# Kernel tuning notes

Hardware: AMD Instinct MI355X
Metric: run time of the kernel (lower is better)

Reference implementation:

```python
import jax, jax.numpy as jnp
import numpy as np

N = 50000      # nodes
E = 800000     # edges (avg degree 16)
F_IN = 256     # in_feats
HID = 64       # hidden_dim (per-head out)
H = 4          # num heads (both layers)
NC = 23        # num_class
NEG_SLOPE = 0.2


def _gat_layer(h, W, attn_l, attn_r, bias, src, dst):
    # h: [N, F_in] -> out: [N, H*HID]; DGL GATConv math (no dropout)
    feat = (h @ W.T).reshape(-1, H, HID)                      # [N,H,D]
    el = jnp.einsum('nhd,hd->nh', feat, attn_l)               # [N,H]
    er = jnp.einsum('nhd,hd->nh', feat, attn_r)               # [N,H]
    e = jax.nn.leaky_relu(el[src] + er[dst], NEG_SLOPE)       # [E,H]
    # edge softmax over incoming edges of each dst node
    m = jax.ops.segment_max(e, dst, num_segments=N)           # [N,H]
    m = jnp.where(jnp.isfinite(m), m, 0.0)
    ex = jnp.exp(e - m[dst])                                  # [E,H]
    den = jax.ops.segment_sum(ex, dst, num_segments=N)        # [N,H]
    a = ex / jnp.maximum(den[dst], 1e-9)                      # [E,H]
    out = jax.ops.segment_sum(a[:, :, None] * feat[src], dst, num_segments=N)  # [N,H,D]
    out = out + bias.reshape(1, H, HID)
    return jax.nn.relu(out).reshape(-1, H * HID)


def setup_inputs() -> dict:
    key = jax.random.key(0)
    ks = jax.random.split(key, 18)
    s = 0.05
    emb = jax.random.normal(ks[4], (NC + 1, F_IN), jnp.float32) * s
    emb = emb.at[NC].set(0.0)  # padding_idx row
    return {
        'features': jax.random.normal(ks[0], (N, F_IN), jnp.float32),
        'input_labels': jax.random.randint(ks[1], (N,), 0, NC + 1),
        'src': jax.random.randint(ks[2], (E,), 0, N),
        'dst': jax.random.randint(ks[3], (E,), 0, N),
        'emb': emb,
        'le_W1': jax.random.normal(ks[5], (4 * F_IN, 2 * F_IN), jnp.float32) * s,
        'le_b1': jnp.zeros((4 * F_IN,), jnp.float32),
        'ln_g': jnp.ones((4 * F_IN,), jnp.float32),
        'ln_b': jnp.zeros((4 * F_IN,), jnp.float32),
        'le_W2': jax.random.normal(ks[6], (F_IN, 4 * F_IN), jnp.float32) * s,
        'le_b2': jnp.zeros((F_IN,), jnp.float32),
        'W1': jax.random.normal(ks[7], (H * HID, F_IN), jnp.float32) * s,
        'al1': jax.random.normal(ks[8], (H, HID), jnp.float32) * s,
        'ar1': jax.random.normal(ks[9], (H, HID), jnp.float32) * s,
        'b1': jnp.zeros((H * HID,), jnp.float32),
        'W2': jax.random.normal(ks[10], (H * HID, H * HID), jnp.float32) * s,
        'al2': jax.random.normal(ks[11], (H, HID), jnp.float32) * s,
        'ar2': jax.random.normal(ks[12], (H, HID), jnp.float32) * s,
        'b2': jnp.zeros((H * HID,), jnp.float32),
    }


def reference(features, emb, le_W1, le_b1, ln_g, ln_b, le_W2, le_b2,
              W1, al1, ar1, b1, W2, al2, ar2, b2,
              input_labels, src, dst):
    # label embedding + 2-layer MLP with LayerNorm (label_embed_layer)
    lab = emb[input_labels]                                   # [N,F_IN]
    x = jnp.concatenate([features, lab], axis=-1)             # [N,2F]
    x = x @ le_W1.T + le_b1                                   # [N,4F]
    mu = jnp.mean(x, axis=-1, keepdims=True)
    var = jnp.var(x, axis=-1, keepdims=True)
    x = (x - mu) * jax.lax.rsqrt(var + 1e-5) * ln_g + ln_b
    x = jax.nn.relu(x)
    h = x @ le_W2.T + le_b2                                   # [N,F_IN]
    h = _gat_layer(h, W1, al1, ar1, b1, src, dst)             # [N,H*HID]
    h = _gat_layer(h, W2, al2, ar2, b2, src, dst)             # [N,H*HID]
    return h
```

## Files before the change

kernel.cpp:

```cpp
#include <hip/hip_runtime.h>
#include <hip/hip_bf16.h>

typedef unsigned short u16;
typedef unsigned int   u32;

#define N_NODES 50000
#define N_EDGES 800000

using s16x8 = __attribute__((ext_vector_type(8))) short;
using f32x4 = __attribute__((ext_vector_type(4))) float;

__device__ __forceinline__ float bf2f(u16 u) {
  u32 x = ((u32)u) << 16;
  return __uint_as_float(x);
}
__device__ __forceinline__ u16 f2bf(float f) {
  u32 x = __float_as_uint(f);
  u32 r = (x + 0x7fffu + ((x >> 16) & 1u)) >> 16;
  return (u16)r;
}
__device__ __forceinline__ s16x8 cvt8_f32(const float* p) {
  const float4 f0 = *reinterpret_cast<const float4*>(p);
  const float4 f1 = *reinterpret_cast<const float4*>(p + 4);
  s16x8 v;
  v[0] = (short)f2bf(f0.x); v[1] = (short)f2bf(f0.y);
  v[2] = (short)f2bf(f0.z); v[3] = (short)f2bf(f0.w);
  v[4] = (short)f2bf(f1.x); v[5] = (short)f2bf(f1.y);
  v[6] = (short)f2bf(f1.z); v[7] = (short)f2bf(f1.w);
  return v;
}

__global__ __launch_bounds__(64)
void detect_dtype(const u16* __restrict__ feats, int* __restrict__ flag)
{
  const int lane = threadIdx.x;
  const u16 u = feats[lane * 2];
  const int ex = (u >> 7) & 0xFF;
  const unsigned long long m = __ballot(ex >= 137);
  if (lane == 0) *flag = (__popcll(m) > 8) ? 1 : 0;
}

template<int DT>
__global__ __launch_bounds__(256)
void conv_weights(const int* __restrict__ flag, int want,
                  const void* p0, const void* p1, const void* p2, const void* p3,
                  const void* p4, const void* p5, const void* p6, const void* p7,
                  const void* p8, const void* p9, const void* p10, const void* p11,
                  const void* p12, const void* p13, u16* __restrict__ arena)
{
  if (*flag != want) return;
  const int gi = blockIdx.x * 256 + threadIdx.x;
  if (gi >= 115296) return;
  const u32 g = (u32)gi * 8;
  const void* src; u32 rel;
  if      (g < 524288) { src = p0;  rel = g; }
  else if (g < 786432) { src = p1;  rel = g - 524288; }
  else if (g < 851968) { src = p2;  rel = g - 786432; }
  else if (g < 917504) { src = p3;  rel = g - 851968; }
  else if (g < 918528) { src = p4;  rel = g - 917504; }
  else if (g < 919552) { src = p5;  rel = g - 918528; }
  else if (g < 920576) { src = p6;  rel = g - 919552; }
  else if (g < 920832) { src = p7;  rel = g - 920576; }
  else if (g < 921088) { src = p8;  rel = g - 920832; }
  else if (g < 921344) { src = p9;  rel = g - 921088; }
  else if (g < 921600) { src = p10; rel = g - 921344; }
  else if (g < 921856) { src = p11; rel = g - 921600; }
  else if (g < 922112) { src = p12; rel = g - 921856; }
  else                 { src = p13; rel = g - 922112; }
  s16x8 v;
  if (DT == 0) v = *reinterpret_cast<const s16x8*>((const u16*)src + rel);
  else         v = cvt8_f32((const float*)src + rel);
  *reinterpret_cast<s16x8*>(arena + g) = v;
}

template<int DT>
__global__ __launch_bounds__(256)
void build_lab(const int* __restrict__ flag, int want,
               const int* __restrict__ labels, const void* __restrict__ emb,
               u16* __restrict__ lab)
{
  if (*flag != want) return;
  const int gi = blockIdx.x * 256 + threadIdx.x;
  if (gi >= N_NODES * 32) return;
  const int row = gi >> 5, c8 = (gi & 31) * 8;
  const int e = labels[row];
  s16x8 v;
  if (DT == 0) v = *reinterpret_cast<const s16x8*>((const u16*)emb + (size_t)e * 256 + c8);
  else         v = cvt8_f32((const float*)emb + (size_t)e * 256 + c8);
  *reinterpret_cast<s16x8*>(lab + (size_t)row * 256 + c8) = v;
}

template<int AMODE>
__global__ __launch_bounds__(256)
void gemm_mfma(const int* __restrict__ flag, int want,
               const u16* __restrict__ A, const u16* __restrict__ Bw,
               const u16* __restrict__ bias, u16* __restrict__ C,
               const u16* __restrict__ featsB, const float* __restrict__ featsF,
               const u16* __restrict__ lab, int M, int N, int K)
{
  if (want >= 0 && *flag != want) return;
  __shared__ u16 As[128 * 64];
  __shared__ u16 Bs[128 * 64];
  const int tid = threadIdx.x;
  const int w = tid >> 6, lane = tid & 63;
  const int wm = w >> 1, wn = w & 1;
  const int bm = blockIdx.x * 128, bn = blockIdx.y * 128;
  const int srow = lane >> 3;
  const int q    = lane & 7;

  f32x4 acc[4][4] = {};

  auto loadA = [&](int k0x, int jj) -> s16x8 {
    const int t  = w * 32 + jj * 8 + srow;
    const int cg = q ^ (t & 7);
    const int kg = k0x + cg * 8;
    const int r  = (bm + t < M) ? bm + t : M - 1;
    if (AMODE == 0)
      return *reinterpret_cast<const s16x8*>(A + (size_t)r * K + kg);
    if (AMODE == 1)
      return (kg < 256)
        ? *reinterpret_cast<const s16x8*>(featsB + (size_t)r * 256 + kg)
        : *reinterpret_cast<const s16x8*>(lab + (size_t)r * 256 + (kg - 256));
    if (kg < 256) return cvt8_f32(featsF + (size_t)r * 256 + kg);
    return *reinterpret_cast<const s16x8*>(lab + (size_t)r * 256 + (kg - 256));
  };
  auto loadB = [&](int k0x, int jj) -> s16x8 {
    const int t  = w * 32 + jj * 8 + srow;
    const int cg = q ^ (t & 7);
    return *reinterpret_cast<const s16x8*>(Bw + (size_t)(bn + t) * K + k0x + cg * 8);
  };

  for (int k0 = 0; k0 < K; k0 += 64) {
    s16x8 ra[4], rb[4];
#pragma unroll
    for (int jj = 0; jj < 4; ++jj) { ra[jj] = loadA(k0, jj); rb[jj] = loadB(k0, jj); }
#pragma unroll
    for (int jj = 0; jj < 4; ++jj) {
      const int t = w * 32 + jj * 8 + srow;
      *reinterpret_cast<s16x8*>(&As[t * 64 + q * 8]) = ra[jj];
      *reinterpret_cast<s16x8*>(&Bs[t * 64 + q * 8]) = rb[jj];
    }
    __syncthreads();
#pragma unroll
    for (int kk = 0; kk < 2; ++kk) {
      s16x8 af[4], bf[4];
#pragma unroll
      for (int i = 0; i < 4; ++i) {
        const int t = wm * 64 + i * 16 + (lane & 15);
        const int c = (kk * 4 + (lane >> 4)) ^ (t & 7);
        af[i] = *reinterpret_cast<const s16x8*>(&As[t * 64 + c * 8]);
      }
#pragma unroll
      for (int j = 0; j < 4; ++j) {
        const int t = wn * 64 + j * 16 + (lane & 15);
        const int c = (kk * 4 + (lane >> 4)) ^ (t & 7);
        bf[j] = *reinterpret_cast<const s16x8*>(&Bs[t * 64 + c * 8]);
      }
#pragma unroll
      for (int i = 0; i < 4; ++i)
#pragma unroll
        for (int j = 0; j < 4; ++j)
          acc[i][j] = __builtin_amdgcn_mfma_f32_16x16x32_bf16(af[i], bf[j], acc[i][j], 0, 0, 0);
    }
    __syncthreads();
  }
#pragma unroll
  for (int j = 0; j < 4; ++j) {
    const int col = bn + wn * 64 + j * 16 + (lane & 15);
    const float bv = bias ? bf2f(bias[col]) : 0.f;
#pragma unroll
    for (int i = 0; i < 4; ++i) {
      const int rbase = bm + wm * 64 + i * 16 + ((lane >> 4) << 2);
#pragma unroll
      for (int r = 0; r < 4; ++r) {
        const int row = rbase + r;
        if (row < M) C[(size_t)row * N + col] = f2bf(acc[i][j][r] + bv);
      }
    }
  }
}

__global__ __launch_bounds__(256)
void ln_relu(u16* __restrict__ y, const u16* __restrict__ g, const u16* __restrict__ b)
{
  const int row = blockIdx.x;
  u16* p = y + (size_t)row * 1024;
  const int t = threadIdx.x;
  const uint2 r = *reinterpret_cast<const uint2*>(p + (t << 2));
  float v[4] = { bf2f((u16)(r.x & 0xffffu)), bf2f((u16)(r.x >> 16)),
                 bf2f((u16)(r.y & 0xffffu)), bf2f((u16)(r.y >> 16)) };
  float s = v[0] + v[1] + v[2] + v[3];
  float qq = v[0]*v[0] + v[1]*v[1] + v[2]*v[2] + v[3]*v[3];
#pragma unroll
  for (int off = 1; off < 64; off <<= 1) { s += __shfl_xor(s, off); qq += __shfl_xor(qq, off); }
  __shared__ float ss[4], sq[4];
  const int w = t >> 6, lane = t & 63;
  if (lane == 0) { ss[w] = s; sq[w] = qq; }
  __syncthreads();
  const float tot  = ss[0] + ss[1] + ss[2] + ss[3];
  const float totq = sq[0] + sq[1] + sq[2] + sq[3];
  const float mu = tot * (1.f / 1024.f);
  const float var = totq * (1.f / 1024.f) - mu * mu;
  const float is = rsqrtf(var + 1e-5f);
  u16 o[4];
#pragma unroll
  for (int i = 0; i < 4; ++i) {
    const int c = (t << 2) + i;
    float val = (v[i] - mu) * is * bf2f(g[c]) + bf2f(b[c]);
    o[i] = f2bf(fmaxf(val, 0.f));
  }
  uint2 wv;
  wv.x = (u32)o[0] | ((u32)o[1] << 16);
  wv.y = (u32)o[2] | ((u32)o[3] << 16);
  *reinterpret_cast<uint2*>(p + (t << 2)) = wv;
}

__global__ __launch_bounds__(256)
void gat_elr(const u16* __restrict__ feat, const u16* __restrict__ al,
             const u16* __restrict__ ar, float* __restrict__ el, float* __restrict__ er)
{
  const int idx = blockIdx.x * 256 + threadIdx.x;
  if (idx >= N_NODES * 4) return;
  const int n = idx >> 2, h = idx & 3;
  const u16* f  = feat + (size_t)n * 256 + h * 64;
  const u16* pl = al + h * 64;
  const u16* pr = ar + h * 64;
  float sl = 0.f, sr = 0.f;
#pragma unroll 8
  for (int d = 0; d < 64; ++d) {
    const float fv = bf2f(f[d]);
    sl = fmaf(fv, bf2f(pl[d]), sl);
    sr = fmaf(fv, bf2f(pr[d]), sr);
  }
  el[idx] = sl; er[idx] = sr;
}

__global__ __launch_bounds__(256)
void edge_scores(const float* __restrict__ el, const float* __restrict__ er,
                 const int* __restrict__ src, const int* __restrict__ dst,
                 float* __restrict__ s)
{
  const int e = blockIdx.x * 256 + threadIdx.x;
  if (e >= N_EDGES) return;
  const float4 l = *reinterpret_cast<const float4*>(el + (size_t)src[e] * 4);
  const float4 r = *reinterpret_cast<const float4*>(er + (size_t)dst[e] * 4);
  float4 o; float x;
  x = l.x + r.x; o.x = x > 0.f ? x : 0.2f * x;
  x = l.y + r.y; o.y = x > 0.f ? x : 0.2f * x;
  x = l.z + r.z; o.z = x > 0.f ? x : 0.2f * x;
  x = l.w + r.w; o.w = x > 0.f ? x : 0.2f * x;
  *reinterpret_cast<float4*>(s + (size_t)e * 4) = o;
}

__global__ __launch_bounds__(256)
void count_edges(const int* __restrict__ dst, int* __restrict__ cnt)
{
  const int e = blockIdx.x * 256 + threadIdx.x;
  if (e < N_EDGES) atomicAdd(&cnt[dst[e]], 1);
}

__global__ __launch_bounds__(64)
void scan_rowptr(const int* __restrict__ cnt, int* __restrict__ rowptr)
{
  const int lane = threadIdx.x;
  int carry = 0;
  if (lane == 0) rowptr[0] = 0;
  for (int base = 0; base < N_NODES; base += 256) {
    const int i0 = base + (lane << 2);
    int4 c = {0, 0, 0, 0};
    if (i0 + 3 < N_NODES) c = *reinterpret_cast<const int4*>(cnt + i0);
    else {
      if (i0 + 0 < N_NODES) c.x = cnt[i0 + 0];
      if (i0 + 1 < N_NODES) c.y = cnt[i0 + 1];
      if (i0 + 2 < N_NODES) c.z = cnt[i0 + 2];
    }
    const int s4 = c.x + c.y + c.z + c.w;
    int v = s4;
#pragma unroll
    for (int off = 1; off < 64; off <<= 1) {
      const int t = __shfl_up(v, off);
      if (lane >= off) v += t;
    }
    const int ex = carry + v - s4;
    const int p1 = ex + c.x, p2 = p1 + c.y, p3 = p2 + c.z, p4 = p3 + c.w;
    if (i0 + 0 < N_NODES) rowptr[i0 + 1] = p1;
    if (i0 + 1 < N_NODES) rowptr[i0 + 2] = p2;
    if (i0 + 2 < N_NODES) rowptr[i0 + 3] = p3;
    if (i0 + 3 < N_NODES) rowptr[i0 + 4] = p4;
    carry += __shfl(v, 63);
  }
}

__global__ __launch_bounds__(256)
void fill_edges(const int* __restrict__ dst, const int* __restrict__ rowptr,
                int* __restrict__ cursor, int* __restrict__ eidx)
{
  const int e = blockIdx.x * 256 + threadIdx.x;
  if (e < N_EDGES) {
    const int d = dst[e];
    const int p = atomicAdd(&cursor[d], 1);
    eidx[rowptr[d] + p] = e;
  }
}

template<int ODT>
__global__ __launch_bounds__(256)
void gat_aggregate(const int* __restrict__ flag, int want,
                   const float* __restrict__ s, const int* __restrict__ rowptr,
                   const int* __restrict__ eidx, const int* __restrict__ src,
                   const u16* __restrict__ feat, const u16* __restrict__ bias,
                   void* __restrict__ out)
{
  if (want >= 0 && *flag != want) return;
  const int lane = threadIdx.x & 63;
  const int node = blockIdx.x * 4 + (threadIdx.x >> 6);
  if (node >= N_NODES) return;
  const int beg = rowptr[node], end = rowptr[node + 1];
  const int deg = end - beg;
  float acc[4] = {0.f, 0.f, 0.f, 0.f};
  if (deg > 0) {
    const int h = lane & 3, j = lane >> 2;
    float mloc = -__builtin_inff();
    for (int i = j; i < deg; i += 16) {
      const int e = eidx[beg + i];
      mloc = fmaxf(mloc, s[(size_t)e * 4 + h]);
    }
#pragma unroll
    for (int off = 4; off < 64; off <<= 1) mloc = fmaxf(mloc, __shfl_xor(mloc, off));
    float dloc = 0.f;
    for (int i = j; i < deg; i += 16) {
      const int e = eidx[beg + i];
      dloc += __expf(s[(size_t)e * 4 + h] - mloc);
    }
#pragma unroll
    for (int off = 4; off < 64; off <<= 1) dloc += __shfl_xor(dloc, off);
    float m_all[4], id_all[4];
#pragma unroll
    for (int hh = 0; hh < 4; ++hh) {
      m_all[hh]  = __shfl(mloc, hh);
      id_all[hh] = 1.f / fmaxf(__shfl(dloc, hh), 1e-9f);
    }
    for (int i = 0; i < deg; ++i) {
      const int e  = eidx[beg + i];
      const int sn = src[e];
      const float4 sv = *reinterpret_cast<const float4*>(s + (size_t)e * 4);
      const u16* frow = feat + (size_t)sn * 256;
      const float a0 = __expf(sv.x - m_all[0]) * id_all[0];
      const float a1 = __expf(sv.y - m_all[1]) * id_all[1];
      const float a2 = __expf(sv.z - m_all[2]) * id_all[2];
      const float a3 = __expf(sv.w - m_all[3]) * id_all[3];
      acc[0] = fmaf(a0, bf2f(frow[lane]),       acc[0]);
      acc[1] = fmaf(a1, bf2f(frow[64 + lane]),  acc[1]);
      acc[2] = fmaf(a2, bf2f(frow[128 + lane]), acc[2]);
      acc[3] = fmaf(a3, bf2f(frow[192 + lane]), acc[3]);
    }
  }
#pragma unroll
  for (int hh = 0; hh < 4; ++hh) {
    const int c = hh * 64 + lane;
    const float v = fmaxf(acc[hh] + bf2f(bias[c]), 0.f);
    if (ODT == 0) ((u16*)out)[(size_t)node * 256 + c] = f2bf(v);
    else          ((float*)out)[(size_t)node * 256 + c] = v;
  }
}

extern "C" void kernel_launch(void* const* d_in, const int* in_sizes, int n_in,
                              void* d_out, int out_size, void* d_ws, size_t ws_size,
                              hipStream_t stream)
{
  const void* features = d_in[0];
  const int* labels    = (const int*)d_in[1];
  const int* src       = (const int*)d_in[2];
  const int* dst       = (const int*)d_in[3];
  const void* emb   = d_in[4];
  const void* le_W1 = d_in[5];
  const void* le_b1 = d_in[6];
  const void* ln_g  = d_in[7];
  const void* ln_b  = d_in[8];
  const void* le_W2 = d_in[9];
  const void* le_b2 = d_in[10];
  const void* W1    = d_in[11];
  const void* al1   = d_in[12];
  const void* ar1   = d_in[13];
  const void* b1    = d_in[14];
  const void* W2    = d_in[15];
  const void* al2   = d_in[16];
  const void* ar2   = d_in[17];
  const void* b2    = d_in[18];

  char* ws = (char*)d_ws;
  u16*   y      = (u16*)(ws + 0);
  u16*   feat   = (u16*)(ws + 0);
  u16*   h2     = (u16*)(ws + 25600000);
  float* el     = (float*)(ws + 51200000);
  float* er     = (float*)(ws + 52000000);
  float* s      = (float*)(ws + 52800000);
  int*   rowptr = (int*)(ws + 65600000);
  int*   cnt    = (int*)(ws + 65800064);
  int*   eidx   = (int*)(ws + 66000128);
  u16*   lab    = (u16*)(ws + 102400000);
  u16*   h      = (u16*)(ws + 102400000);
  u16*   arena  = (u16*)(ws + 128000000);
  int*   flag   = (int*)(ws + 129844736);

  u16* aleW1 = arena + 0;
  u16* aleW2 = arena + 524288;
  u16* aW1   = arena + 786432;
  u16* aW2   = arena + 851968;
  u16* aleb1 = arena + 917504;
  u16* alng  = arena + 918528;
  u16* alnb  = arena + 919552;
  u16* aleb2 = arena + 920576;
  u16* aal1  = arena + 920832;
  u16* aar1  = arena + 921088;
  u16* ab1   = arena + 921344;
  u16* aal2  = arena + 921600;
  u16* aar2  = arena + 921856;
  u16* ab2   = arena + 922112;

  detect_dtype<<<1, 64, 0, stream>>>((const u16*)features, flag);

  conv_weights<0><<<451, 256, 0, stream>>>(flag, 0, le_W1, le_W2, W1, W2, le_b1, ln_g,
                                           ln_b, le_b2, al1, ar1, b1, al2, ar2, b2, arena);
  conv_weights<1><<<451, 256, 0, stream>>>(flag, 1, le_W1, le_W2, W1, W2, le_b1, ln_g,
                                           ln_b, le_b2, al1, ar1, b1, al2, ar2, b2, arena);
  build_lab<0><<<6250, 256, 0, stream>>>(flag, 0, labels, emb, lab);
  build_lab<1><<<6250, 256, 0, stream>>>(flag, 1, labels, emb, lab);

  gemm_mfma<1><<<dim3(391, 8), 256, 0, stream>>>(flag, 0, nullptr, aleW1, aleb1, y,
                                                 (const u16*)features, nullptr, lab,
                                                 N_NODES, 1024, 512);
  gemm_mfma<2><<<dim3(391, 8), 256, 0, stream>>>(flag, 1, nullptr, aleW1, aleb1, y,
                                                 nullptr, (const float*)features, lab,
                                                 N_NODES, 1024, 512);
  ln_relu<<<N_NODES, 256, 0, stream>>>(y, alng, alnb);
  gemm_mfma<0><<<dim3(391, 2), 256, 0, stream>>>(flag, -1, y, aleW2, aleb2, h,
                                                 nullptr, nullptr, nullptr,
                                                 N_NODES, 256, 1024);

  hipMemsetAsync(cnt, 0, N_NODES * 4, stream);
  count_edges<<<N_EDGES / 256, 256, 0, stream>>>(dst, cnt);
  scan_rowptr<<<1, 64, 0, stream>>>(cnt, rowptr);
  hipMemsetAsync(cnt, 0, N_NODES * 4, stream);
  fill_edges<<<N_EDGES / 256, 256, 0, stream>>>(dst, rowptr, cnt, eidx);

  gemm_mfma<0><<<dim3(391, 2), 256, 0, stream>>>(flag, -1, h, aW1, nullptr, feat,
                                                 nullptr, nullptr, nullptr,
                                                 N_NODES, 256, 256);
  gat_elr<<<782, 256, 0, stream>>>(feat, aal1, aar1, el, er);
  edge_scores<<<N_EDGES / 256, 256, 0, stream>>>(el, er, src, dst, s);
  gat_aggregate<0><<<12500, 256, 0, stream>>>(flag, -1, s, rowptr, eidx, src, feat, ab1, h2);

  gemm_mfma<0><<<dim3(391, 2), 256, 0, stream>>>(flag, -1, h2, aW2, nullptr, feat,
                                                 nullptr, nullptr, nullptr,
                                                 N_NODES, 256, 256);
  gat_elr<<<782, 256, 0, stream>>>(feat, aal2, aar2, el, er);
  edge_scores<<<N_EDGES / 256, 256, 0, stream>>>(el, er, src, dst, s);
  gat_aggregate<0><<<12500, 256, 0, stream>>>(flag, 0, s, rowptr, eidx, src, feat, ab2, d_out);
  gat_aggregate<1><<<12500, 256, 0, stream>>>(flag, 1, s, rowptr, eidx, src, feat, ab2, d_out);
}
```

Baseline: 942.0 us.

## Aggregate each node with a whole block, online softmax and split edges across wavefronts

Measured after the change: 994.2 us. 5.5% more time.

```diff
diff --git a/kernel.cpp b/kernel.cpp
--- a/kernel.cpp
+++ b/kernel.cpp
@@ -312,56 +312,69 @@
                    void* __restrict__ out)
 {
   if (want >= 0 && *flag != want) return;
-  const int lane = threadIdx.x & 63;
-  const int node = blockIdx.x * 4 + (threadIdx.x >> 6);
-  if (node >= N_NODES) return;
-  const int beg = rowptr[node], end = rowptr[node + 1];
-  const int deg = end - beg;
+  const int node = blockIdx.x;
+  const int tid  = threadIdx.x;
+  const int w    = tid >> 6, lane = tid & 63;
+  const int beg  = rowptr[node];
+  const int deg  = rowptr[node + 1] - beg;
+
+  __shared__ float sm_m[4][4], sm_d[4][4];
+  __shared__ float sm_acc[4][256];
+
   float acc[4] = {0.f, 0.f, 0.f, 0.f};
+  const float NEG = -1e30f;
+
   if (deg > 0) {
     const int h = lane & 3, j = lane >> 2;
-    float mloc = -__builtin_inff();
-    for (int i = j; i < deg; i += 16) {
+    float mloc = NEG, dloc = 0.f;
+    for (int i = w * 16 + j; i < deg; i += 64) {
       const int e = eidx[beg + i];
-      mloc = fmaxf(mloc, s[(size_t)e * 4 + h]);
-    }
-#pragma unroll
-    for (int off = 4; off < 64; off <<= 1) mloc = fmaxf(mloc, __shfl_xor(mloc, off));
-    float dloc = 0.f;
-    for (int i = j; i < deg; i += 16) {
-      const int e = eidx[beg + i];
-      dloc += __expf(s[(size_t)e * 4 + h] - mloc);
-    }
-#pragma unroll
-    for (int off = 4; off < 64; off <<= 1) dloc += __shfl_xor(dloc, off);
+      const float sv = s[(size_t)e * 4 + h];
+      const float mn = fmaxf(mloc, sv);
+      dloc = dloc * __expf(mloc - mn) + __expf(sv - mn);
+      mloc = mn;
+    }
+#pragma unroll
+    for (int off = 4; off < 64; off <<= 1) {
+      const float mo = __shfl_xor(mloc, off);
+      const float dd = __shfl_xor(dloc, off);
+      const float mn = fmaxf(mloc, mo);
+      dloc = dloc * __expf(mloc - mn) + dd * __expf(mo - mn);
+      mloc = mn;
+    }
+    if (lane < 4) { sm_m[w][lane] = mloc; sm_d[w][lane] = dloc; }
+    __syncthreads();
     float m_all[4], id_all[4];
 #pragma unroll
     for (int hh = 0; hh < 4; ++hh) {
-      m_all[hh]  = __shfl(mloc, hh);
-      id_all[hh] = 1.f / fmaxf(__shfl(dloc, hh), 1e-9f);
-    }
-    for (int i = 0; i < deg; ++i) {
+      float m = fmaxf(fmaxf(sm_m[0][hh], sm_m[1][hh]), fmaxf(sm_m[2][hh], sm_m[3][hh]));
+      float d = sm_d[0][hh] * __expf(sm_m[0][hh] - m) + sm_d[1][hh] * __expf(sm_m[1][hh] - m)
+              + sm_d[2][hh] * __expf(sm_m[2][hh] - m) + sm_d[3][hh] * __expf(sm_m[3][hh] - m);
+      m_all[hh]  = m;
+      id_all[hh] = 1.f / fmaxf(d, 1e-9f);
+    }
+    const int hme = lane >> 4;
+    const int c0  = lane * 4;
+    const float mh = m_all[hme], idh = id_all[hme];
+    for (int i = w; i < deg; i += 4) {
       const int e  = eidx[beg + i];
       const int sn = src[e];
-      const float4 sv = *reinterpret_cast<const float4*>(s + (size_t)e * 4);
-      const u16* frow = feat + (size_t)sn * 256;
-      const float a0 = __expf(sv.x - m_all[0]) * id_all[0];
-      const float a1 = __expf(sv.y - m_all[1]) * id_all[1];
-      const float a2 = __expf(sv.z - m_all[2]) * id_all[2];
-      const float a3 = __expf(sv.w - m_all[3]) * id_all[3];
-      acc[0] = fmaf(a0, bf2f(frow[lane]),       acc[0]);
-      acc[1] = fmaf(a1, bf2f(frow[64 + lane]),  acc[1]);
-      acc[2] = fmaf(a2, bf2f(frow[128 + lane]), acc[2]);
-      acc[3] = fmaf(a3, bf2f(frow[192 + lane]), acc[3]);
-    }
-  }
-#pragma unroll
-  for (int hh = 0; hh < 4; ++hh) {
-    const int c = hh * 64 + lane;
-    const float v = fmaxf(acc[hh] + bf2f(bias[c]), 0.f);
-    if (ODT == 0) ((u16*)out)[(size_t)node * 256 + c] = f2bf(v);
-    else          ((float*)out)[(size_t)node * 256 + c] = v;
-  }
+      const float a = __expf(s[(size_t)e * 4 + hme] - mh) * idh;
+      const uint2 f4 = *reinterpret_cast<const uint2*>(feat + (size_t)sn * 256 + c0);
+      acc[0] = fmaf(a, bf2f((u16)(f4.x & 0xffffu)), acc[0]);
+      acc[1] = fmaf(a, bf2f((u16)(f4.x >> 16)),     acc[1]);
+      acc[2] = fmaf(a, bf2f((u16)(f4.y & 0xffffu)), acc[2]);
+      acc[3] = fmaf(a, bf2f((u16)(f4.y >> 16)),     acc[3]);
+    }
+  } else {
+    __syncthreads();
+  }
+  *reinterpret_cast<float4*>(&sm_acc[w][lane * 4]) = make_float4(acc[0], acc[1], acc[2], acc[3]);
+  __syncthreads();
+  const float v = fmaxf(sm_acc[0][tid] + sm_acc[1][tid] + sm_acc[2][tid] + sm_acc[3][tid]
+                        + bf2f(bias[tid]), 0.f);
+  if (ODT == 0) ((u16*)out)[(size_t)node * 256 + tid] = f2bf(v);
+  else          ((float*)out)[(size_t)node * 256 + tid] = v;
 }
 
 extern "C" void kernel_launch(void* const* d_in, const int* in_sizes, int n_in,
@@ -449,13 +462,13 @@
                                                  N_NODES, 256, 256);
   gat_elr<<<782, 256, 0, stream>>>(feat, aal1, aar1, el, er);
   edge_scores<<<N_EDGES / 256, 256, 0, stream>>>(el, er, src, dst, s);
-  gat_aggregate<0><<<12500, 256, 0, stream>>>(flag, -1, s, rowptr, eidx, src, feat, ab1, h2);
+  gat_aggregate<0><<<N_NODES, 256, 0, stream>>>(flag, -1, s, rowptr, eidx, src, feat, ab1, h2);
 
   gemm_mfma<0><<<dim3(391, 2), 256, 0, stream>>>(flag, -1, h2, aW2, nullptr, feat,
                                                  nullptr, nullptr, nullptr,
                                                  N_NODES, 256, 256);
   gat_elr<<<782, 256, 0, stream>>>(feat, aal2, aar2, el, er);
   edge_scores<<<N_EDGES / 256, 256, 0, stream>>>(el, er, src, dst, s);
-  gat_aggregate<0><<<12500, 256, 0, stream>>>(flag, 0, s, rowptr, eidx, src, feat, ab2, d_out);
-  gat_aggregate<1><<<12500, 256, 0, stream>>>(flag, 1, s, rowptr, eidx, src, feat, ab2, d_out);
-}
+  gat_aggregate<0><<<N_NODES, 256, 0, stream>>>(flag, 0, s, rowptr, eidx, src, feat, ab2, d_out);
+  gat_aggregate<1><<<N_NODES, 256, 0, stream>>>(flag, 1, s, rowptr, eidx, src, feat, ab2, d_out);
+}
```
